# Optimization experiments

Hardware: AMD Instinct MI355X
Metric: run time of the kernel (lower is better)

Reference implementation:

```python
import jax, jax.numpy as jnp
import numpy as np

# Screen config (matches init_kwargs)
W, H, TL = 1920, 1080, 16
NBW = -(-W // TL)          # 120
NBH = -(-H // TL)          # 68
NB = NBW * NBH             # 8160 tiles
N = 500_000                # number of points
K = 5                      # max tiles per axis a point can overlap (radius < 24, TL=16)
RADIUS_MAX = 24.0


def setup_inputs() -> dict:
    key = jax.random.key(0)
    k1, k2, k3 = jax.random.split(key, 3)
    pos2d = jax.random.uniform(k1, (N, 2), dtype=jnp.float32) * jnp.array([W, H], dtype=jnp.float32)
    radius = jax.random.uniform(k2, (N,), dtype=jnp.float32) * (RADIUS_MAX - 1.0) + 1.0
    depth = jax.random.normal(k3, (N,), dtype=jnp.float32)
    return {"pos2d": pos2d, "radius": radius, "depth": depth}


def reference(pos2d, radius, depth):
    # Tile bounds per point (identical clamping semantics to the torch module).
    xmin = jnp.clip(jnp.floor_divide(pos2d[:, 0] - radius, TL), 0, NBW).astype(jnp.int32)
    ymin = jnp.clip(jnp.floor_divide(pos2d[:, 1] - radius, TL), 0, NBH).astype(jnp.int32)
    xmax = jnp.clip(jnp.floor_divide(pos2d[:, 0] + radius, TL) + 1, 0, NBW).astype(jnp.int32)
    ymax = jnp.clip(jnp.floor_divide(pos2d[:, 1] + radius, TL) + 1, 0, NBH).astype(jnp.int32)

    # Enumerate a fixed KxK candidate tile window per point, mask out-of-range tiles.
    dxy = jnp.arange(K, dtype=jnp.int32)
    xi = xmin[:, None] + dxy            # [N, K]
    yi = ymin[:, None] + dxy            # [N, K]
    vx = xi < xmax[:, None]
    vy = yi < ymax[:, None]
    valid = (vx[:, :, None] & vy[:, None, :]).reshape(-1)              # [E]
    tid = (xi[:, :, None] * NBH + yi[:, None, :]).reshape(-1)          # [E] flat tile id (x-major, as in module)
    tid = jnp.where(valid, tid, NB).astype(jnp.int32)                  # sentinel NB -> sorts to end
    pid = jnp.broadcast_to(jnp.arange(N, dtype=jnp.int32)[:, None, None], (N, K, K)).reshape(-1)
    d_entry = jnp.broadcast_to(depth[:, None, None], (N, K, K)).reshape(-1)

    # Counting-sort equivalent: per-tile histogram + exclusive cumsum offsets.
    counts = jax.ops.segment_sum(valid.astype(jnp.int32), tid, num_segments=NB + 1)[:NB]
    tile_count = jnp.concatenate([jnp.zeros((1,), jnp.int32), jnp.cumsum(counts)[:-1].astype(jnp.int32)])

    # Sort pairs by (tile id, depth descending) -> contiguous per-tile, depth-sorted index lists.
    order = jnp.lexsort((-d_entry, tid))
    tid_s = tid[order]
    pid_s = pid[order]
    live = tid_s < NB
    tile_indices = jnp.where(live, pid_s, -1)                          # padded with -1 at the tail
    sorted_depth = jnp.where(live, depth[pid_s], 0.0)                  # depths in per-tile sorted order
    return tile_count, tile_indices, sorted_depth
```

## Files before the change

kernel.cpp:

```cpp
#include <hip/hip_runtime.h>
#include <stdint.h>
#include <math.h>

typedef unsigned short u16;
typedef unsigned int u32;
typedef unsigned long long u64;

#define NBW 120
#define NBH 68
#define NTILES (NBW * NBH)
#define NPTS 500000
#define EE 12500000
#define SORT_CAP 768
#define NBKT 512
#define CAP 128
#define SLABF (NTILES * CAP * 2)
#define HB2 128
#define HT2 512
#define DX 121
#define DY 69
#define DCELLS 8352
#define DCW (DCELLS / 2)

__device__ __forceinline__ int clampi(int v, int lo, int hi) {
    return v < lo ? lo : (v > hi ? hi : v);
}

__device__ __forceinline__ void tile_window(float x, float y, float r,
                                            int& x0, int& x1, int& y0, int& y1) {
    x0 = clampi((int)floorf((x - r) * 0.0625f), 0, NBW);
    x1 = clampi((int)floorf((x + r) * 0.0625f) + 1, 0, NBW);
    y0 = clampi((int)floorf((y - r) * 0.0625f), 0, NBH);
    y1 = clampi((int)floorf((y + r) * 0.0625f) + 1, 0, NBH);
}

__device__ __forceinline__ u32 depth_key(float d) {
    u32 fu = __float_as_uint(d);
    u32 asc = (fu & 0x80000000u) ? ~fu : (fu | 0x80000000u);
    return ~asc;
}
__device__ __forceinline__ float depth_unkey(u32 dk) {
    u32 asc = ~dk;
    u32 fu = (asc & 0x80000000u) ? (asc & 0x7FFFFFFFu) : ~asc;
    return __uint_as_float(fu);
}

__device__ __forceinline__ int tile_of_block(int b) {
    return (b & 7) * (NTILES / 8) + (b >> 3);
}

__device__ __forceinline__ u32 bucket_of(u32 dk, const u32* __restrict__ Ts) {
    u32 k = dk >> 24;
    u32 t0 = Ts[k], t1 = Ts[k + 1];
    u32 b = t0 + (((t1 - t0) * ((dk >> 8) & 0xFFFFu)) >> 16);
    return b >= NBKT ? (NBKT - 1) : b;
}

__device__ __forceinline__ void lds_inc16(u32* arr, int cell) {
    atomicAdd(&arr[cell >> 1], (cell & 1) ? 0x10000u : 1u);
}


__global__ void zero_cnt_kernel(u32* __restrict__ cnt) {
    int i = blockIdx.x * 1024 + threadIdx.x;
    if (i < NTILES) cnt[i] = 0;
}

__global__ __launch_bounds__(HT2) void scatter_hist_kernel(const float2* __restrict__ pos,
                                                           const float* __restrict__ rad,
                                                           const float* __restrict__ depth,
                                                           u32* __restrict__ cnt,
                                                           u64* __restrict__ slab,
                                                           u32* __restrict__ diffslc) {
    __shared__ u32 s_dp[DCW];
    __shared__ u32 s_dm[DCW];
    int tid = threadIdx.x;
    for (int w = tid; w < DCW; w += HT2) { s_dp[w] = 0; s_dm[w] = 0; }
    __syncthreads();

    for (int i = blockIdx.x * HT2 + tid; i < NPTS; i += HB2 * HT2) {
        float2 p = pos[i];
        float r = rad[i];
        int x0, x1, y0, y1;
        tile_window(p.x, p.y, r, x0, x1, y0, y1);
        int cx = (int)(p.x * 0.0625f);
        int cy = (int)(p.y * 0.0625f);
        u32 dk = depth_key(depth[i]);
        u32 meta = ((u32)(cx - x0) << 11) | ((u32)(x1 - cx - 1) << 9)
                 | ((u32)y0 << 2) | (u32)(y1 - y0 - 1);
        int ct = cx * NBH + cy;
        u32 slot = atomicAdd(&cnt[ct], 1u);
        if (slot < CAP)
            slab[(size_t)ct * CAP + slot] = ((u64)dk << 32) | ((u64)(u32)i << 13) | (u64)meta;
        lds_inc16(s_dp, x0 * DY + y0);
        lds_inc16(s_dp, x1 * DY + y1);
        lds_inc16(s_dm, x0 * DY + y1);
        lds_inc16(s_dm, x1 * DY + y0);
    }
    __syncthreads();

    for (int wi = tid; wi < DCW; wi += HT2) {
        u32 pw = s_dp[wi], mw = s_dm[wi];
        int d0 = (int)(pw & 0xFFFFu) - (int)(mw & 0xFFFFu);
        int d1 = (int)(pw >> 16)     - (int)(mw >> 16);
        diffslc[blockIdx.x * DCW + wi] = ((u32)d0 & 0xFFFFu) | ((u32)d1 << 16);
    }
}

__global__ void reduce_diff_kernel(const u32* __restrict__ diffslc, int* __restrict__ sdg) {
    int c = blockIdx.x * 256 + threadIdx.x;
    if (c >= DCELLS) return;
    int wi = c >> 1, sh = (c & 1) * 16;
    int acc = 0;
    for (int b = 0; b < HB2; ++b)
        acc += (int)(short)((diffslc[b * DCW + wi] >> sh) & 0xFFFFu);
    sdg[c] = acc;
}

__global__ __launch_bounds__(1024) void scan2_kernel(const int* __restrict__ sdg,
                                                     u32* __restrict__ eo,
                                                     float* __restrict__ out_count,
                                                     u32* __restrict__ Tg) {
    __shared__ u32 sA[1024], sB[1024];
    __shared__ int sd[DCELLS];
    __shared__ u32 traw[257];
    int t = threadIdx.x;
    int base = t * 8;

    if (blockIdx.x == 0) {
        for (int c = t; c < DCELLS; c += 1024) sd[c] = sdg[c];
        __syncthreads();
        if (t < DX) { int run = 0; for (int y = 0; y < DY; ++y) { run += sd[t * DY + y]; sd[t * DY + y] = run; } }
        __syncthreads();
        if (t < DY) { int run = 0; for (int x = 0; x < DX; ++x) { run += sd[x * DY + t]; sd[x * DY + t] = run; } }
        __syncthreads();

        u32 local[8]; u32 sum = 0;
#pragma unroll
        for (int j = 0; j < 8; ++j) {
            int idx = base + j;
            u32 c = 0;
            if (idx < NTILES) {
                int x = idx / NBH, y = idx % NBH;
                c = (u32)sd[x * DY + y];
            }
            local[j] = c; sum += c;
        }
        sA[t] = sum;
        __syncthreads();
        u32 *cur = sA, *nxt = sB;
        for (int off = 1; off < 1024; off <<= 1) {
            u32 v = cur[t];
            if (t >= off) v += cur[t - off];
            nxt[t] = v;
            __syncthreads();
            u32* tmp = cur; cur = nxt; nxt = tmp;
        }
        u32 run = cur[t] - sum;
#pragma unroll
        for (int j = 0; j < 8; ++j) {
            int idx = base + j;
            if (idx < NTILES) {
                eo[idx] = run;
                out_count[idx] = (float)run;
                run += local[j];
            }
        }
        if (t == 1023) eo[NTILES] = cur[1023];
    } else {
        if (t < 257) {
            u32 dkb = (u32)t << 24;
            float d = depth_unkey(dkb);
            float u;
            if (d != d) u = (t < 128) ? 0.f : 1.f;
            else {
                float dc = fminf(fmaxf(d, -12.f), 12.f);
                u = 0.5f * erfcf(dc * 0.70710678f);
            }
            traw[t] = (u32)(u * (float)NBKT + 0.5f);
        }
        __syncthreads();
        if (t == 0) {
            u32 run = 0;
            for (int k = 0; k < 257; ++k) {
                u32 v = traw[k];
                if (v > NBKT) v = NBKT;
                if (v > run) run = v;
                Tg[k] = run;
            }
        }
    }
}

__global__ __launch_bounds__(256) void tile_build_kernel(const u32* __restrict__ cnt,
                                                         const u64* __restrict__ slab,
                                                         const u32* __restrict__ eo,
                                                         const u32* __restrict__ Tg,
                                                         float* __restrict__ out_idx,
                                                         float* __restrict__ out_depth) {
    __shared__ u64 keys[SORT_CAP];
    __shared__ u64 keys2[SORT_CAP];
    __shared__ u32 boff[NBKT + 1];
    __shared__ u32 bcur[NBKT];
    __shared__ u32 Ts[257];
    __shared__ u32 wsum[4];
    __shared__ u32 lcnt;
    __shared__ u32 nb_off[26];
    __shared__ u32 nb_base[25];
    __shared__ int nb_dcx[25];

    int tid = threadIdx.x;
    int lane = tid & 63;
    int wv = tid >> 6;

    {
        u32 total = eo[NTILES];
        u32 tailn = EE - total;
        u32 per = (tailn + NTILES - 1) / NTILES;
        u64 s = (u64)total + (u64)blockIdx.x * per;
        u64 e = s + per; if (e > (u64)EE) e = EE;
        for (u64 i = s + tid; i < e; i += 256) out_idx[i] = -1.f;

        u32 limit = EE - SLABF;
        u32 tn2 = limit > total ? limit - total : 0;
        u32 per2 = (tn2 + NTILES - 1) / NTILES;
        u64 s2 = (u64)total + (u64)blockIdx.x * per2;
        u64 e2 = s2 + per2; if (e2 > (u64)limit) e2 = limit;
        for (u64 i = s2 + tid; i < e2; i += 256) out_depth[i] = 0.f;
    }

    int t = tile_of_block(blockIdx.x);
    u32 base = eo[t];
    int cnt_e = (int)(eo[t + 1] - base);
    if (cnt_e <= 0) return;

    int tx = t / NBH;
    int ty = t % NBH;
    bool big = cnt_e > SORT_CAP;

    for (int b = tid; b < NBKT; b += 256) boff[b] = 0;
    for (int k = tid; k < 257; k += 256) Ts[k] = Tg[k];
    if (tid == 0) lcnt = 0;
    if (tid < 25) {
        int dx = tid / 5 - 2, dy = tid % 5 - 2;
        int ncx = tx + dx, ncy = ty + dy;
        u32 n = 0, b = 0;
        if (ncx >= 0 && ncx < NBW && ncy >= 0 && ncy < NBH) {
            int nt = ncx * NBH + ncy;
            n = cnt[nt]; if (n > CAP) n = CAP;
            b = (u32)nt * CAP;
        }
        nb_base[tid] = b;
        nb_dcx[tid] = dx;
        nb_off[tid + 1] = n;
    }
    if (tid == 25) nb_off[0] = 0;
    __syncthreads();
    if (tid == 0) {
        u32 run = 0;
#pragma unroll
        for (int k = 1; k <= 25; ++k) { run += nb_off[k]; nb_off[k] = run; }
    }
    __syncthreads();
    u32 S = nb_off[25];

    if (!big) {
        for (u32 j = tid; j < S; j += 256) {
            int lo = 0, hi = 24;
            while (lo < hi) {
                int mid = (lo + hi + 1) >> 1;
                if (nb_off[mid] <= j) lo = mid; else hi = mid - 1;
            }
            u64 v = slab[nb_base[lo] + (j - nb_off[lo])];
            u32 meta = (u32)v & 0x1FFFu;
            int h = (int)(meta & 3u);
            int y0 = (int)((meta >> 2) & 127u);
            int dx1m1 = (int)((meta >> 9) & 3u);
            int dx0 = (int)((meta >> 11) & 3u);
            int dcx = nb_dcx[lo];
            if (dx0 >= dcx && dx1m1 >= -dcx && ty >= y0 && ty <= y0 + h) {
                u32 slot = atomicAdd(&lcnt, 1u);
                keys[slot] = v;
                atomicAdd(&boff[bucket_of((u32)(v >> 32), Ts)], 1u);
            }
        }
        __syncthreads();

        {
            int b0 = tid * 2;
            u32 h0 = boff[b0], h1 = boff[b0 + 1];
            u32 tsum = h0 + h1;
            u32 v = tsum;
            for (int off = 1; off < 64; off <<= 1) {
                u32 n = __shfl_up(v, off, 64);
                if (lane >= off) v += n;
            }
            if (lane == 63) wsum[wv] = v;
            __syncthreads();
            u32 wpre = 0;
            for (int w = 0; w < wv; ++w) wpre += wsum[w];
            u32 run = wpre + v - tsum;
            boff[b0] = run;     bcur[b0] = run;     run += h0;
            boff[b0 + 1] = run; bcur[b0 + 1] = run; run += h1;
            if (tid == 255) boff[NBKT] = run;
        }
        __syncthreads();

        for (int i = tid; i < cnt_e; i += 256) {
            u64 v = keys[i];
            u32 slot = atomicAdd(&bcur[bucket_of((u32)(v >> 32), Ts)], 1u);
            keys2[slot] = v;
        }
        __syncthreads();

        for (int b = tid; b < NBKT; b += 256) {
            int s = (int)boff[b], e = (int)boff[b + 1];
            for (int i = s + 1; i < e; ++i) {
                u64 k = keys2[i];
                int j = i - 1;
                while (j >= s && keys2[j] > k) { keys2[j + 1] = keys2[j]; --j; }
                keys2[j + 1] = k;
            }
        }
        __syncthreads();

        for (int i = tid; i < cnt_e; i += 256) {
            u64 k = keys2[i];
            u32 pid = (u32)(k >> 13) & 0x7FFFFu;
            u32 dk  = (u32)(k >> 32);
            out_idx[base + i]   = (float)pid;
            out_depth[base + i] = depth_unkey(dk);
        }
    } else {
        for (u32 j = tid; j < S; j += 256) {
            int lo = 0, hi = 24;
            while (lo < hi) {
                int mid = (lo + hi + 1) >> 1;
                if (nb_off[mid] <= j) lo = mid; else hi = mid - 1;
            }
            u64 v = slab[nb_base[lo] + (j - nb_off[lo])];
            u32 meta = (u32)v & 0x1FFFu;
            int h = (int)(meta & 3u);
            int y0 = (int)((meta >> 2) & 127u);
            int dx1m1 = (int)((meta >> 9) & 3u);
            int dx0 = (int)((meta >> 11) & 3u);
            int dcx = nb_dcx[lo];
            if (dx0 >= dcx && dx1m1 >= -dcx && ty >= y0 && ty <= y0 + h) {
                u32 pid = (u32)(v >> 13) & 0x7FFFFu;
                u32 dk  = (u32)(v >> 32);
                u32 slot = atomicAdd(&lcnt, 1u);
                out_idx[base + slot] = (float)pid;
                out_depth[base + slot] = depth_unkey(dk);
            }
        }
        __syncthreads();
        for (int round = 0; round < cnt_e; ++round) {
            for (int i = (round & 1) + 2 * tid; i + 1 < cnt_e; i += 512) {
                float fi0 = out_idx[base + i], fi1 = out_idx[base + i + 1];
                float fd0 = out_depth[base + i], fd1 = out_depth[base + i + 1];
                u64 k0 = ((u64)depth_key(fd0) << 19) | (u64)(u32)fi0;
                u64 k1 = ((u64)depth_key(fd1) << 19) | (u64)(u32)fi1;
                if (k0 > k1) {
                    out_idx[base + i] = fi1; out_idx[base + i + 1] = fi0;
                    out_depth[base + i] = fd1; out_depth[base + i + 1] = fd0;
                }
            }
            __syncthreads();
        }
    }
}

__global__ void zero_slab_kernel(float4* __restrict__ dst) {
    int n = SLABF / 4;
    for (int i = blockIdx.x * 256 + threadIdx.x; i < n; i += 512 * 256)
        dst[i] = make_float4(0.f, 0.f, 0.f, 0.f);
}

extern "C" void kernel_launch(void* const* d_in, const int* in_sizes, int n_in,
                              void* d_out, int out_size, void* d_ws, size_t ws_size,
                              hipStream_t stream) {
    (void)in_sizes; (void)n_in; (void)out_size; (void)ws_size;

    const float2* pos  = (const float2*)d_in[0];
    const float* rad   = (const float*)d_in[1];
    const float* depth = (const float*)d_in[2];

    float* out        = (float*)d_out;
    float* out_count  = out;
    float* out_idx    = out + NTILES;
    float* out_depth  = out + NTILES + EE;

    u32* cnt     = (u32*)d_ws;
    u32* eo      = cnt + NTILES;
    int* sdg     = (int*)(eo + NTILES + 1);
    u32* Tg      = (u32*)(sdg + DCELLS);
    u32* diffslc = Tg + 257;

    u64* slab = (u64*)(out_depth + EE) - (size_t)NTILES * CAP;

    zero_cnt_kernel<<<8, 1024, 0, stream>>>(cnt);
    scatter_hist_kernel<<<HB2, HT2, 0, stream>>>(pos, rad, depth, cnt, slab, diffslc);
    reduce_diff_kernel<<<(DCELLS + 255) / 256, 256, 0, stream>>>(diffslc, sdg);
    scan2_kernel<<<2, 1024, 0, stream>>>(sdg, eo, out_count, Tg);
    tile_build_kernel<<<NTILES, 256, 0, stream>>>(cnt, slab, eo, Tg, out_idx, out_depth);
    zero_slab_kernel<<<512, 256, 0, stream>>>((float4*)(out_depth + EE - SLABF));
}
```

Before: 206.0 us.

## Parallelize diff reduction with atomics and walk neighbor slabs per wave

The scatter-histogram grid grows to 256 blocks of 1024 threads. Its per-block diff slices now live in the tail of the output buffer instead of the workspace. The diff reduction is split into chunks across more blocks that combine their partial sums into a pre-zeroed sdg with atomics. In tile_build, the flat loop over concatenated neighbor slabs, which needed a prefix sum and a binary search per element, is replaced by each wave walking whole neighbor slabs directly. This removes the search and one barrier, but a wave may now leave lanes idle on short neighbor lists.

```diff
diff --git a/kernel.cpp b/kernel.cpp
--- a/kernel.cpp
+++ b/kernel.cpp
@@ -15,8 +15,10 @@
 #define NBKT 512
 #define CAP 128
 #define SLABF (NTILES * CAP * 2)
-#define HB2 128
-#define HT2 512
+#define HB2 256
+#define HT2 1024
+#define RD_CH 8
+#define RD_WB 17
 #define DX 121
 #define DY 69
 #define DCELLS 8352
@@ -61,9 +63,11 @@
 }
 
 
-__global__ void zero_cnt_kernel(u32* __restrict__ cnt) {
+__global__ void zero_kernel(u32* __restrict__ cnt, int* __restrict__ sdg) {
     int i = blockIdx.x * 1024 + threadIdx.x;
     if (i < NTILES) cnt[i] = 0;
+    int j = i - NTILES;
+    if (j >= 0 && j < DCELLS) sdg[j] = 0;
 }
 
 __global__ __launch_bounds__(HT2) void scatter_hist_kernel(const float2* __restrict__ pos,
@@ -108,13 +112,19 @@
 }
 
 __global__ void reduce_diff_kernel(const u32* __restrict__ diffslc, int* __restrict__ sdg) {
-    int c = blockIdx.x * 256 + threadIdx.x;
-    if (c >= DCELLS) return;
-    int wi = c >> 1, sh = (c & 1) * 16;
-    int acc = 0;
-    for (int b = 0; b < HB2; ++b)
-        acc += (int)(short)((diffslc[b * DCW + wi] >> sh) & 0xFFFFu);
-    sdg[c] = acc;
+    int chunk = blockIdx.x / RD_WB;
+    int wb    = blockIdx.x % RD_WB;
+    int wi = wb * 256 + threadIdx.x;
+    if (wi >= DCW) return;
+    int a0 = 0, a1 = 0;
+    int b0 = chunk * (HB2 / RD_CH);
+    for (int b = b0; b < b0 + HB2 / RD_CH; ++b) {
+        u32 w = diffslc[b * DCW + wi];
+        a0 += (int)(short)(w & 0xFFFFu);
+        a1 += (int)(short)(w >> 16);
+    }
+    atomicAdd(&sdg[2 * wi],     a0);
+    atomicAdd(&sdg[2 * wi + 1], a1);
 }
 
 __global__ __launch_bounds__(1024) void scan2_kernel(const int* __restrict__ sdg,
@@ -205,7 +215,7 @@
     __shared__ u32 Ts[257];
     __shared__ u32 wsum[4];
     __shared__ u32 lcnt;
-    __shared__ u32 nb_off[26];
+    __shared__ u32 nb_n[25];
     __shared__ u32 nb_base[25];
     __shared__ int nb_dcx[25];
 
@@ -252,36 +262,28 @@
         }
         nb_base[tid] = b;
         nb_dcx[tid] = dx;
-        nb_off[tid + 1] = n;
-    }
-    if (tid == 25) nb_off[0] = 0;
+        nb_n[tid] = n;
+    }
     __syncthreads();
-    if (tid == 0) {
-        u32 run = 0;
-#pragma unroll
-        for (int k = 1; k <= 25; ++k) { run += nb_off[k]; nb_off[k] = run; }
-    }
-    __syncthreads();
-    u32 S = nb_off[25];
 
     if (!big) {
-        for (u32 j = tid; j < S; j += 256) {
-            int lo = 0, hi = 24;
-            while (lo < hi) {
-                int mid = (lo + hi + 1) >> 1;
-                if (nb_off[mid] <= j) lo = mid; else hi = mid - 1;
-            }
-            u64 v = slab[nb_base[lo] + (j - nb_off[lo])];
-            u32 meta = (u32)v & 0x1FFFu;
-            int h = (int)(meta & 3u);
-            int y0 = (int)((meta >> 2) & 127u);
-            int dx1m1 = (int)((meta >> 9) & 3u);
-            int dx0 = (int)((meta >> 11) & 3u);
-            int dcx = nb_dcx[lo];
-            if (dx0 >= dcx && dx1m1 >= -dcx && ty >= y0 && ty <= y0 + h) {
-                u32 slot = atomicAdd(&lcnt, 1u);
-                keys[slot] = v;
-                atomicAdd(&boff[bucket_of((u32)(v >> 32), Ts)], 1u);
+        for (int k = wv; k < 25; k += 4) {
+            u32 n = nb_n[k];
+            if (!n) continue;
+            const u64* sp = slab + nb_base[k];
+            int dcx = nb_dcx[k];
+            for (u32 j = lane; j < n; j += 64) {
+                u64 v = sp[j];
+                u32 meta = (u32)v & 0x1FFFu;
+                int h = (int)(meta & 3u);
+                int y0 = (int)((meta >> 2) & 127u);
+                int dx1m1 = (int)((meta >> 9) & 3u);
+                int dx0 = (int)((meta >> 11) & 3u);
+                if (dx0 >= dcx && dx1m1 >= -dcx && ty >= y0 && ty <= y0 + h) {
+                    u32 slot = atomicAdd(&lcnt, 1u);
+                    keys[slot] = v;
+                    atomicAdd(&boff[bucket_of((u32)(v >> 32), Ts)], 1u);
+                }
             }
         }
         __syncthreads();
@@ -332,25 +334,25 @@
             out_depth[base + i] = depth_unkey(dk);
         }
     } else {
-        for (u32 j = tid; j < S; j += 256) {
-            int lo = 0, hi = 24;
-            while (lo < hi) {
-                int mid = (lo + hi + 1) >> 1;
-                if (nb_off[mid] <= j) lo = mid; else hi = mid - 1;
-            }
-            u64 v = slab[nb_base[lo] + (j - nb_off[lo])];
-            u32 meta = (u32)v & 0x1FFFu;
-            int h = (int)(meta & 3u);
-            int y0 = (int)((meta >> 2) & 127u);
-            int dx1m1 = (int)((meta >> 9) & 3u);
-            int dx0 = (int)((meta >> 11) & 3u);
-            int dcx = nb_dcx[lo];
-            if (dx0 >= dcx && dx1m1 >= -dcx && ty >= y0 && ty <= y0 + h) {
-                u32 pid = (u32)(v >> 13) & 0x7FFFFu;
-                u32 dk  = (u32)(v >> 32);
-                u32 slot = atomicAdd(&lcnt, 1u);
-                out_idx[base + slot] = (float)pid;
-                out_depth[base + slot] = depth_unkey(dk);
+        for (int k = wv; k < 25; k += 4) {
+            u32 n = nb_n[k];
+            if (!n) continue;
+            const u64* sp = slab + nb_base[k];
+            int dcx = nb_dcx[k];
+            for (u32 j = lane; j < n; j += 64) {
+                u64 v = sp[j];
+                u32 meta = (u32)v & 0x1FFFu;
+                int h = (int)(meta & 3u);
+                int y0 = (int)((meta >> 2) & 127u);
+                int dx1m1 = (int)((meta >> 9) & 3u);
+                int dx0 = (int)((meta >> 11) & 3u);
+                if (dx0 >= dcx && dx1m1 >= -dcx && ty >= y0 && ty <= y0 + h) {
+                    u32 pid = (u32)(v >> 13) & 0x7FFFFu;
+                    u32 dk  = (u32)(v >> 32);
+                    u32 slot = atomicAdd(&lcnt, 1u);
+                    out_idx[base + slot] = (float)pid;
+                    out_depth[base + slot] = depth_unkey(dk);
+                }
             }
         }
         __syncthreads();
@@ -394,13 +396,13 @@
     u32* eo      = cnt + NTILES;
     int* sdg     = (int*)(eo + NTILES + 1);
     u32* Tg      = (u32*)(sdg + DCELLS);
-    u32* diffslc = Tg + 257;
-
-    u64* slab = (u64*)(out_depth + EE) - (size_t)NTILES * CAP;
-
-    zero_cnt_kernel<<<8, 1024, 0, stream>>>(cnt);
+
+    u64* slab    = (u64*)(out_depth + EE) - (size_t)NTILES * CAP;
+    u32* diffslc = (u32*)(out_idx + EE) - (size_t)HB2 * DCW;
+
+    zero_kernel<<<(NTILES + DCELLS + 1023) / 1024, 1024, 0, stream>>>(cnt, sdg);
     scatter_hist_kernel<<<HB2, HT2, 0, stream>>>(pos, rad, depth, cnt, slab, diffslc);
-    reduce_diff_kernel<<<(DCELLS + 255) / 256, 256, 0, stream>>>(diffslc, sdg);
+    reduce_diff_kernel<<<RD_CH * RD_WB, 256, 0, stream>>>(diffslc, sdg);
     scan2_kernel<<<2, 1024, 0, stream>>>(sdg, eo, out_count, Tg);
     tile_build_kernel<<<NTILES, 256, 0, stream>>>(cnt, slab, eo, Tg, out_idx, out_depth);
     zero_slab_kernel<<<512, 256, 0, stream>>>((float4*)(out_depth + EE - SLABF));
```

Result: faster. 196.3 us (-4.7%).
